# Kernel optimization log

Hardware: AMD Instinct MI355X
Metric: run time of the kernel (lower is better)

Reference implementation:

```python
import jax, jax.numpy as jnp
import numpy as np

EMBED_DIM = 1024
NUM_HEADS = 16
HEAD_DIM = EMBED_DIM // NUM_HEADS


def setup_inputs() -> dict:
    key = jax.random.key(0)
    ks = jax.random.split(key, 5)
    B, S, D = 2, 2048, EMBED_DIM
    scale = 1.0 / np.sqrt(D)
    x = jax.random.normal(ks[0], (B, S, D), dtype=jnp.float32)
    qkv_w = jax.random.uniform(ks[1], (3 * D, D), dtype=jnp.float32, minval=-scale, maxval=scale)
    qkv_b = jax.random.uniform(ks[2], (3 * D,), dtype=jnp.float32, minval=-scale, maxval=scale)
    out_w = jax.random.uniform(ks[3], (D, D), dtype=jnp.float32, minval=-scale, maxval=scale)
    out_b = jax.random.uniform(ks[4], (D,), dtype=jnp.float32, minval=-scale, maxval=scale)
    return {"x": x, "qkv_w": qkv_w, "qkv_b": qkv_b, "out_w": out_w, "out_b": out_b}


def reference(x, qkv_w, qkv_b, out_w, out_b):
    B, S, D = x.shape
    H, hd = NUM_HEADS, HEAD_DIM
    # QKV projection (torch Linear: y = x @ W^T + b)
    qkv = jnp.einsum('bsd,ed->bse', x, qkv_w) + qkv_b          # [B,S,3D]
    qkv = qkv.reshape(B, S, 3, H, hd)
    q, k, v = (jnp.moveaxis(qkv[:, :, i], 2, 1) for i in range(3))  # each [B,H,S,hd]
    scores = jnp.einsum('bhqd,bhkd->bhqk', q, k) / np.sqrt(hd)  # [B,H,S,S]
    probs = jax.nn.softmax(scores, axis=-1)
    attn = jnp.einsum('bhqk,bhkd->bhqd', probs, v)              # [B,H,S,hd]
    attn = jnp.moveaxis(attn, 1, 2).reshape(B, S, D)
    return jnp.einsum('bsd,ed->bse', attn, out_w) + out_b
```

## Files before the change

### kernel.cpp

```cpp
#include <hip/hip_runtime.h>
#include <stdint.h>

typedef __bf16 bf16;
typedef __attribute__((ext_vector_type(2))) __bf16 bf16x2;
typedef __attribute__((ext_vector_type(4))) __bf16 bf16x4;
typedef __attribute__((ext_vector_type(8))) __bf16 bf16x8;
typedef __attribute__((ext_vector_type(4))) float f32x4;
typedef __attribute__((ext_vector_type(16))) float f32x16;
typedef __attribute__((ext_vector_type(4))) short short4v;

#define LOG2E_OVER_8 0.18033688011112042f

#if __has_builtin(__builtin_amdgcn_exp2f)
#define EXP2(x) __builtin_amdgcn_exp2f(x)
#else
#define EXP2(x) exp2f(x)
#endif

__device__ __forceinline__ void gl_lds16(const bf16* g, bf16* l) {
  __builtin_amdgcn_global_load_lds(
      (const __attribute__((address_space(1))) void*)g,
      (__attribute__((address_space(3))) void*)l, 16, 0, 0);
}
#define WAIT_VM0_BARRIER() asm volatile("s_waitcnt vmcnt(0)\n\ts_barrier" ::: "memory")

__device__ __forceinline__ uint32_t pack2(float a, float b) {
  union { bf16x2 v; uint32_t u; } z;
  z.v[0] = (bf16)a; z.v[1] = (bf16)b;
  return z.u;
}

#define N_X  (4096 * 1024)
#define N_WQ (3072 * 1024)
#define N_WO (1024 * 1024)
__global__ __launch_bounds__(256) void cvt3_kernel(const float* __restrict__ x,
                                                   const float* __restrict__ wq,
                                                   const float* __restrict__ wo,
                                                   bf16* __restrict__ d) {
  int i = (blockIdx.x * 256 + threadIdx.x) * 8;
  const float* s;
  if (i < N_X) s = x + i;
  else if (i < N_X + N_WQ) s = wq + (i - N_X);
  else s = wo + (i - N_X - N_WQ);
  float4 a = *(const float4*)s;
  float4 b = *(const float4*)(s + 4);
  bf16x8 o;
  o[0] = (bf16)a.x; o[1] = (bf16)a.y; o[2] = (bf16)a.z; o[3] = (bf16)a.w;
  o[4] = (bf16)b.x; o[5] = (bf16)b.y; o[6] = (bf16)b.z; o[7] = (bf16)b.w;
  *(bf16x8*)(d + i) = o;
}

template <int EPI>
__global__ __launch_bounds__(256, 3) void gemm_bt(
    const bf16* __restrict__ A, const bf16* __restrict__ Bw,
    const float* __restrict__ bias,
    bf16* __restrict__ qo, bf16* __restrict__ ko, bf16* __restrict__ vTo,
    float* __restrict__ outF) {
  constexpr int MT = EPI ? 64 : 128;
  constexpr int MI = MT / 32;
  constexpr int ASZ = MT * 32;
  constexpr int BSZ = 128 * 32;
  constexpr int RS = 136;
  constexpr int SME = EPI ? (2 * ASZ + 2 * BSZ) : (128 * RS);
  __shared__ __attribute__((aligned(16))) bf16 smem[SME];

  int bx, by;
  {
    const int f = blockIdx.x;
    const int xcd = f & 7, idx = f >> 3;
    if constexpr (EPI == 0) { by = xcd * 4 + (idx & 3); bx = idx >> 2; }
    else                    { by = xcd * 8 + (idx & 7); bx = idx >> 3; }
  }

  const int t = threadIdx.x;
  const int L = t & 63;
  const int li = L & 15;
  const int qd = L >> 4;
  const int w = t >> 6;
  const int wm = (w >> 1) * (MT / 2);
  const int wn = (w & 1) * 64;
  const int bm0 = by * MT;
  const int bn0 = bx * 128;
  const int r_st = t >> 2;
  const int c_st = (t & 3) * 8;

  const bf16* Ab = A + (size_t)bm0 * 1024;
  const bf16* Bb = Bw + (size_t)bn0 * 1024;

  auto issue = [&](int k0, int bi) {
    bf16* As_ = smem + bi * ASZ;
    bf16* Bs_ = smem + 2 * ASZ + bi * BSZ;
    gl_lds16(Ab + (size_t)r_st * 1024 + k0 + c_st, As_ + t * 8);
    if constexpr (MT == 128)
      gl_lds16(Ab + (size_t)(r_st + 64) * 1024 + k0 + c_st, As_ + (t + 256) * 8);
    gl_lds16(Bb + (size_t)r_st * 1024 + k0 + c_st, Bs_ + t * 8);
    gl_lds16(Bb + (size_t)(r_st + 64) * 1024 + k0 + c_st, Bs_ + (t + 256) * 8);
  };

  f32x4 acc[MI][4] = {};
  issue(0, 0);
  for (int it = 0; it < 32; ++it) {
    WAIT_VM0_BARRIER();
    if (it < 31) issue((it + 1) * 32, (it + 1) & 1);
    const bf16* Ac = smem + (it & 1) * ASZ;
    const bf16* Bc = smem + 2 * ASZ + (it & 1) * BSZ;
    bf16x8 af[MI], bfr[4];
#pragma unroll
    for (int mi = 0; mi < MI; ++mi)
      af[mi] = *(const bf16x8*)(Ac + (wm + mi * 16 + li) * 32 + qd * 8);
#pragma unroll
    for (int ni = 0; ni < 4; ++ni)
      bfr[ni] = *(const bf16x8*)(Bc + (wn + ni * 16 + li) * 32 + qd * 8);
#pragma unroll
    for (int mi = 0; mi < MI; ++mi)
#pragma unroll
      for (int ni = 0; ni < 4; ++ni)
        acc[mi][ni] = __builtin_amdgcn_mfma_f32_16x16x32_bf16(af[mi], bfr[ni],
                                                              acc[mi][ni], 0, 0, 0);
  }

  if constexpr (EPI == 0) {
    const int which = bn0 >> 10;
    __syncthreads();
    bf16* Ct = smem;
    if (which == 2) {
#pragma unroll
      for (int mi = 0; mi < MI; ++mi) {
        const int m_l = wm + mi * 16 + qd * 4;
#pragma unroll
        for (int ni = 0; ni < 4; ++ni) {
          const int n_l = wn + ni * 16 + li;
          const float bi = bias[bn0 + n_l];
          bf16x4 pk;
#pragma unroll
          for (int r = 0; r < 4; ++r) pk[r] = (bf16)(acc[mi][ni][r] + bi);
          *(bf16x4*)(Ct + n_l * RS + m_l) = pk;
        }
      }
    } else {
      const float sc = (which == 0) ? LOG2E_OVER_8 : 1.0f;
#pragma unroll
      for (int mi = 0; mi < MI; ++mi) {
        const int m_l = wm + mi * 16 + qd * 4;
#pragma unroll
        for (int ni = 0; ni < 4; ++ni) {
          const int n_l = wn + ni * 16 + li;
          const float bi = bias[bn0 + n_l];
#pragma unroll
          for (int r = 0; r < 4; ++r)
            Ct[(m_l + r) * RS + n_l] = (bf16)((acc[mi][ni][r] + bi) * sc);
        }
      }
    }
    __syncthreads();
    const int jr = t >> 4;
    const int jc = t & 15;
#pragma unroll
    for (int pass = 0; pass < 8; ++pass) {
      const int row = pass * 16 + jr;
      bf16x8 vv = *(const bf16x8*)(Ct + row * RS + jc * 8);
      if (which == 2) {
        const int n_g = bn0 + row;
        const int hh = (n_g >> 6) & 15, dd = n_g & 63;
        const int bb = bm0 >> 11;
        const int s_b = (bm0 & 2047) + jc * 8;
        *(bf16x8*)(vTo + ((size_t)(bb * 16 + hh) * 64 + dd) * 2048 + s_b) = vv;
      } else {
        const int m_g = bm0 + row;
        const int bb = m_g >> 11, ss = m_g & 2047;
        const int n_g = bn0 + jc * 8;
        const int hh = (n_g >> 6) & 15, dd = n_g & 63;
        bf16* dst = (which == 0 ? qo : ko);
        *(bf16x8*)(dst + ((size_t)(bb * 16 + hh) * 2048 + ss) * 64 + dd) = vv;
      }
    }
  } else {
#pragma unroll
    for (int mi = 0; mi < MI; ++mi) {
      const int m_g = bm0 + wm + mi * 16 + qd * 4;
#pragma unroll
      for (int ni = 0; ni < 4; ++ni) {
        const int n_g = bn0 + wn + ni * 16 + li;
        const float bi = bias[n_g];
#pragma unroll
        for (int r = 0; r < 4; ++r)
          outF[(size_t)(m_g + r) * 1024 + n_g] = acc[mi][ni][r] + bi;
      }
    }
  }
}

__global__ __launch_bounds__(128, 2) void attn_fwd(
    const bf16* __restrict__ Q, const bf16* __restrict__ K,
    const bf16* __restrict__ VT, bf16* __restrict__ AO) {
  __shared__ __attribute__((aligned(16))) bf16 Ks[2 * 4096];
  __shared__ __attribute__((aligned(16))) bf16 Vs[2 * 4096];
  const int t = threadIdx.x;
  const int L = t & 63;
  const int m31 = L & 31;
  const int hi = L >> 5;
  const int w = t >> 6;

  const int lid = blockIdx.x;
  const int bh_ = ((lid & 7) << 2) + (lid >> 8);
  const int qb = (lid >> 3) & 31;
  const int b = bh_ >> 4, h = bh_ & 15;
  const size_t bh = (size_t)(b * 16 + h);

  const bf16* Qp = Q + bh * 2048 * 64;
  const bf16* Kp = K + bh * 2048 * 64;
  const bf16* Vp = VT + bh * 64 * 2048;
  const int q0 = qb * 64 + w * 32;

  bf16x8 qf[4];
#pragma unroll
  for (int s = 0; s < 4; ++s)
    qf[s] = *(const bf16x8*)(Qp + (size_t)(q0 + m31) * 64 + s * 16 + hi * 8);

  f32x16 acc[2] = {};
  float lsum = 0.f;

  const int srow = t >> 3;
  const int scc = (t & 7) ^ (srow & 7);
  auto issue = [&](int kt, int bi) {
    const bf16* Kt = Kp + (size_t)kt * 4096;
    const bf16* Vt = Vp + kt * 64;
    bf16* Kd = Ks + bi * 4096;
    bf16* Vd = Vs + bi * 4096;
#pragma unroll
    for (int r = 0; r < 4; ++r) {
      gl_lds16(Kt + (srow + 16 * r) * 64 + scc * 8, Kd + (t + 128 * r) * 8);
      gl_lds16(Vt + (size_t)(srow + 16 * r) * 2048 + scc * 8, Vd + (t + 128 * r) * 8);
    }
  };

  const int rlow = m31 & 7;
  issue(0, 0);
  for (int kt = 0; kt < 32; ++kt) {
    WAIT_VM0_BARRIER();
    if (kt < 31) issue(kt + 1, (kt + 1) & 1);
    const bf16* Kc = Ks + (kt & 1) * 4096;
    const bf16* Vc = Vs + (kt & 1) * 4096;

    f32x16 st[2];
#pragma unroll
    for (int kt2 = 0; kt2 < 2; ++kt2) {
      f32x16 z = {};
#pragma unroll
      for (int s = 0; s < 4; ++s) {
        bf16x8 kf = *(const bf16x8*)(
            Kc + ((kt2 * 32 + m31) * 8 + ((2 * s + hi) ^ rlow)) * 8);
        z = __builtin_amdgcn_mfma_f32_32x32x16_bf16(kf, qf[s], z, 0, 0, 0);
      }
      st[kt2] = z;
    }

#pragma unroll
    for (int kt2 = 0; kt2 < 2; ++kt2)
#pragma unroll
      for (int u = 0; u < 4; ++u) {
        float e0 = EXP2(st[kt2][4 * u]);
        float e1 = EXP2(st[kt2][4 * u + 1]);
        float e2 = EXP2(st[kt2][4 * u + 2]);
        float e3 = EXP2(st[kt2][4 * u + 3]);
        lsum += (e0 + e1) + (e2 + e3);
        union { uint32_t uu[2]; short4v s4; } pk;
        pk.uu[0] = pack2(e0, e1);
        pk.uu[1] = pack2(e2, e3);
        const int g = kt2 * 4 + u;
#pragma unroll
        for (int dt = 0; dt < 2; ++dt) {
          short4v vf = *(const short4v*)(
              Vc + ((dt * 32 + m31) * 8 + (g ^ rlow)) * 8 + hi * 4);
          acc[dt] = __builtin_amdgcn_mfma_f32_32x32x8bf16_1k(pk.s4, vf,
                                                             acc[dt], 0, 0, 0);
        }
      }
  }

  lsum += __shfl_xor(lsum, 32);
  const float inv = 1.f / lsum;

#pragma unroll
  for (int r = 0; r < 16; ++r) {
    const int qrow = (r & 3) + 8 * (r >> 2) + 4 * hi;
    const float invq = __shfl(inv, qrow);
    const size_t base = ((size_t)b * 2048 + q0 + qrow) * 1024 + h * 64 + m31;
    AO[base] = (bf16)(acc[0][r] * invq);
    AO[base + 32] = (bf16)(acc[1][r] * invq);
  }
}

extern "C" void kernel_launch(void* const* d_in, const int* in_sizes, int n_in,
                              void* d_out, int out_size, void* d_ws, size_t ws_size,
                              hipStream_t stream) {
  const float* x = (const float*)d_in[0];
  const float* qkvw = (const float*)d_in[1];
  const float* qkvb = (const float*)d_in[2];
  const float* outw = (const float*)d_in[3];
  const float* outb = (const float*)d_in[4];
  float* out = (float*)d_out;

  bf16* xb = (bf16*)d_ws;
  bf16* wq = xb + (size_t)N_X;
  bf16* wo = wq + (size_t)N_WQ;
  bf16* q = wo + (size_t)N_WO;
  bf16* kk = q + (size_t)2 * 16 * 2048 * 64;
  bf16* vT = kk + (size_t)2 * 16 * 2048 * 64;
  bf16* attn = xb;

  cvt3_kernel<<<4096, 256, 0, stream>>>(x, qkvw, outw, xb);

  gemm_bt<0><<<768, 256, 0, stream>>>(xb, wq, qkvb, q, kk, vT, nullptr);
  attn_fwd<<<1024, 128, 0, stream>>>(q, kk, vT, attn);
  gemm_bt<1><<<512, 256, 0, stream>>>(attn, wo, outb, nullptr, nullptr, nullptr, out);
}
```

Baseline: 194.2 us.

## Load K tiles straight into registers and give each wave private V buffers

The attention kernel no longer stages K through shared memory. Each wave loads its K fragments from global memory into double-buffered registers, one step ahead. V is still staged through LDS, but each wave now has its own double-buffered region and waits with a vmcnt count instead of a block-wide barrier. This removes the cross-wave barrier and the LDS round-trip for K, at the cost of more VGPRs, duplicate K loads from both waves, and reliance on the manual vmcnt(16) count being correct alongside the compiler's own waits.

```diff
diff --git a/kernel.cpp b/kernel.cpp
--- a/kernel.cpp
+++ b/kernel.cpp
@@ -193,8 +193,7 @@
 __global__ __launch_bounds__(128, 2) void attn_fwd(
     const bf16* __restrict__ Q, const bf16* __restrict__ K,
     const bf16* __restrict__ VT, bf16* __restrict__ AO) {
-  __shared__ __attribute__((aligned(16))) bf16 Ks[2 * 4096];
-  __shared__ __attribute__((aligned(16))) bf16 Vs[2 * 4096];
+  __shared__ __attribute__((aligned(16))) bf16 Vs[2 * 8192];
   const int t = threadIdx.x;
   const int L = t & 63;
   const int m31 = L & 31;
@@ -219,42 +218,41 @@
 
   f32x16 acc[2] = {};
   float lsum = 0.f;
-
-  const int srow = t >> 3;
-  const int scc = (t & 7) ^ (srow & 7);
-  auto issue = [&](int kt, int bi) {
-    const bf16* Kt = Kp + (size_t)kt * 4096;
+  const int rlow = m31 & 7;
+
+  bf16* Vw = Vs + w * 8192;
+  const int vd = L >> 3;
+  const int vc = (L & 7) ^ vd;
+  auto issueV = [&](int kt, int bi) {
     const bf16* Vt = Vp + kt * 64;
-    bf16* Kd = Ks + bi * 4096;
-    bf16* Vd = Vs + bi * 4096;
-#pragma unroll
-    for (int r = 0; r < 4; ++r) {
-      gl_lds16(Kt + (srow + 16 * r) * 64 + scc * 8, Kd + (t + 128 * r) * 8);
-      gl_lds16(Vt + (size_t)(srow + 16 * r) * 2048 + scc * 8, Vd + (t + 128 * r) * 8);
-    }
+    bf16* dst = Vw + bi * 4096 + L * 8;
+#pragma unroll
+    for (int r = 0; r < 8; ++r)
+      gl_lds16(Vt + (size_t)(r * 8 + vd) * 2048 + vc * 8, dst + r * 512);
   };
 
-  const int rlow = m31 & 7;
-  issue(0, 0);
-  for (int kt = 0; kt < 32; ++kt) {
-    WAIT_VM0_BARRIER();
-    if (kt < 31) issue(kt + 1, (kt + 1) & 1);
-    const bf16* Kc = Ks + (kt & 1) * 4096;
-    const bf16* Vc = Vs + (kt & 1) * 4096;
-
+  auto step = [&](int kt, bf16x8* kc, bf16x8* kn) {
+    const int bi = kt & 1;
+    if (kt < 31) {
+      issueV(kt + 1, bi ^ 1);
+#pragma unroll
+      for (int i = 0; i < 8; ++i)
+        kn[i] = *(const bf16x8*)(Kp +
+            (size_t)((kt + 1) * 64 + (i >> 2) * 32 + m31) * 64 +
+            (i & 3) * 16 + hi * 8);
+    }
     f32x16 st[2];
 #pragma unroll
     for (int kt2 = 0; kt2 < 2; ++kt2) {
       f32x16 z = {};
 #pragma unroll
-      for (int s = 0; s < 4; ++s) {
-        bf16x8 kf = *(const bf16x8*)(
-            Kc + ((kt2 * 32 + m31) * 8 + ((2 * s + hi) ^ rlow)) * 8);
-        z = __builtin_amdgcn_mfma_f32_32x32x16_bf16(kf, qf[s], z, 0, 0, 0);
-      }
+      for (int s = 0; s < 4; ++s)
+        z = __builtin_amdgcn_mfma_f32_32x32x16_bf16(kc[kt2 * 4 + s], qf[s], z,
+                                                    0, 0, 0);
       st[kt2] = z;
     }
-
+    asm volatile("s_waitcnt vmcnt(16)" ::: "memory");
+    const bf16* Vc = Vw + bi * 4096;
 #pragma unroll
     for (int kt2 = 0; kt2 < 2; ++kt2)
 #pragma unroll
@@ -276,6 +274,17 @@
                                                              acc[dt], 0, 0, 0);
         }
       }
+  };
+
+  issueV(0, 0);
+  bf16x8 ka[8], kb[8];
+#pragma unroll
+  for (int i = 0; i < 8; ++i)
+    ka[i] = *(const bf16x8*)(Kp + (size_t)((i >> 2) * 32 + m31) * 64 +
+                             (i & 3) * 16 + hi * 8);
+  for (int kt = 0; kt < 32; kt += 2) {
+    step(kt, ka, kb);
+    step(kt + 1, kb, ka);
   }
 
   lsum += __shfl_xor(lsum, 32);
```

After: 208.4 us. +7.3%, slower.

## Load V tiles directly into registers instead of staging through LDS

Applied to the files above, without the earlier changes.

The attention kernel stops staging V tiles in shared memory. Each lane now loads its V fragments straight from global memory into a double-buffered register array, prefetched one tile ahead. Only K still goes through async global-to-LDS copies, and the barrier wait becomes vmcnt(16) so the in-flight V register loads are not waited on. This removes the V LDS writes and reads and halves LDS usage, but costs about 64 extra VGPRs and uses narrow, strided 8-byte global loads that may coalesce poorly.

```diff
diff --git a/kernel.cpp b/kernel.cpp
--- a/kernel.cpp
+++ b/kernel.cpp
@@ -23,6 +23,8 @@
       (__attribute__((address_space(3))) void*)l, 16, 0, 0);
 }
 #define WAIT_VM0_BARRIER() asm volatile("s_waitcnt vmcnt(0)\n\ts_barrier" ::: "memory")
+#define WAIT_VMN_BARRIER(N) \
+  asm volatile("s_waitcnt vmcnt(" #N ")\n\ts_barrier" ::: "memory")
 
 __device__ __forceinline__ uint32_t pack2(float a, float b) {
   union { bf16x2 v; uint32_t u; } z;
@@ -194,7 +196,6 @@
     const bf16* __restrict__ Q, const bf16* __restrict__ K,
     const bf16* __restrict__ VT, bf16* __restrict__ AO) {
   __shared__ __attribute__((aligned(16))) bf16 Ks[2 * 4096];
-  __shared__ __attribute__((aligned(16))) bf16 Vs[2 * 4096];
   const int t = threadIdx.x;
   const int L = t & 63;
   const int m31 = L & 31;
@@ -219,28 +220,35 @@
 
   f32x16 acc[2] = {};
   float lsum = 0.f;
+  const int rlow = m31 & 7;
 
   const int srow = t >> 3;
   const int scc = (t & 7) ^ (srow & 7);
-  auto issue = [&](int kt, int bi) {
+  auto issueK = [&](int kt, int bi) {
     const bf16* Kt = Kp + (size_t)kt * 4096;
-    const bf16* Vt = Vp + kt * 64;
     bf16* Kd = Ks + bi * 4096;
-    bf16* Vd = Vs + bi * 4096;
-#pragma unroll
-    for (int r = 0; r < 4; ++r) {
+#pragma unroll
+    for (int r = 0; r < 4; ++r)
       gl_lds16(Kt + (srow + 16 * r) * 64 + scc * 8, Kd + (t + 128 * r) * 8);
-      gl_lds16(Vt + (size_t)(srow + 16 * r) * 2048 + scc * 8, Vd + (t + 128 * r) * 8);
-    }
   };
 
-  const int rlow = m31 & 7;
-  issue(0, 0);
-  for (int kt = 0; kt < 32; ++kt) {
-    WAIT_VM0_BARRIER();
-    if (kt < 31) issue(kt + 1, (kt + 1) & 1);
+  const bf16* Vrow0 = Vp + (size_t)m31 * 2048 + hi * 4;
+  auto loadV = [&](int kt, short4v* vr) {
+#pragma unroll
+    for (int g = 0; g < 8; ++g)
+#pragma unroll
+      for (int dt = 0; dt < 2; ++dt)
+        vr[g * 2 + dt] =
+            *(const short4v*)(Vrow0 + (size_t)dt * 32 * 2048 + kt * 64 + g * 8);
+  };
+
+  auto step = [&](int kt, short4v* vcur, short4v* vnext) {
+    WAIT_VMN_BARRIER(16);
+    if (kt < 31) {
+      issueK(kt + 1, (kt + 1) & 1);
+      loadV(kt + 1, vnext);
+    }
     const bf16* Kc = Ks + (kt & 1) * 4096;
-    const bf16* Vc = Vs + (kt & 1) * 4096;
 
     f32x16 st[2];
 #pragma unroll
@@ -269,13 +277,18 @@
         pk.uu[1] = pack2(e2, e3);
         const int g = kt2 * 4 + u;
 #pragma unroll
-        for (int dt = 0; dt < 2; ++dt) {
-          short4v vf = *(const short4v*)(
-              Vc + ((dt * 32 + m31) * 8 + (g ^ rlow)) * 8 + hi * 4);
-          acc[dt] = __builtin_amdgcn_mfma_f32_32x32x8bf16_1k(pk.s4, vf,
-                                                             acc[dt], 0, 0, 0);
-        }
-      }
+        for (int dt = 0; dt < 2; ++dt)
+          acc[dt] = __builtin_amdgcn_mfma_f32_32x32x8bf16_1k(
+              pk.s4, vcur[g * 2 + dt], acc[dt], 0, 0, 0);
+      }
+  };
+
+  short4v va[16], vb[16];
+  issueK(0, 0);
+  loadV(0, va);
+  for (int kt = 0; kt < 32; kt += 2) {
+    step(kt, va, vb);
+    step(kt + 1, vb, va);
   }
 
   lsum += __shfl_xor(lsum, 32);
```

Result: slower. 257.0 us (+32.3%).
